# Kernel optimization log

Measured on AMD Instinct MI355X. Metric: run time of the kernel, lower is better.

Reference implementation:

```python
import jax, jax.numpy as jnp
import numpy as np

D_MODEL = 512
NUM_HEADS = 8
DFF = 2048
EPS = 1e-5


def _layernorm(x, gamma, beta):
    mu = jnp.mean(x, axis=-1, keepdims=True)
    var = jnp.mean(jnp.square(x - mu), axis=-1, keepdims=True)
    return (x - mu) / jnp.sqrt(var + EPS) * gamma + beta


def _mha(xq, xkv, wq, bq, wk, bk, wv, bv, wo, bo, mask):
    B, Sq, D = xq.shape
    Sk = xkv.shape[1]
    H = NUM_HEADS
    depth = D // H
    q = (xq @ wq + bq).reshape(B, Sq, H, depth).transpose(0, 2, 1, 3)  # bhqd
    k = (xkv @ wk + bk).reshape(B, Sk, H, depth).transpose(0, 2, 1, 3)  # bhkd
    v = (xkv @ wv + bv).reshape(B, Sk, H, depth).transpose(0, 2, 1, 3)  # bhkd
    logits = jnp.einsum('bhqd,bhkd->bhqk', q, k) / jnp.sqrt(jnp.float32(depth))
    if mask is not None:
        logits = logits + mask * -10000.0
    attn = jax.nn.softmax(logits, axis=-1)  # [B,H,Sq,Sk]
    out = jnp.einsum('bhqk,bhkd->bhqd', attn, v)
    out = out.transpose(0, 2, 1, 3).reshape(B, Sq, D)
    return out @ wo + bo, attn


def setup_inputs() -> dict:
    key = jax.random.key(0)
    ks = jax.random.split(key, 32)
    B, T, S, D, F = 8, 1024, 1024, D_MODEL, DFF
    sd = 1.0 / np.sqrt(D)
    inp = {
        'x': jax.random.normal(ks[0], (B, T, D), jnp.float32),
        'enc_output': jax.random.normal(ks[1], (B, S, D), jnp.float32),
        # causal mask: 1 where attention is disallowed (future positions)
        'look_ahead_mask': (1.0 - jnp.tril(jnp.ones((T, T), jnp.float32)))[None, None],
        'padding_mask': jnp.zeros((1, 1, 1, S), jnp.float32),
    }
    i = 2
    for pfx in ('1', '2'):
        for nm in ('wq', 'wk', 'wv', 'wo'):
            inp[nm + pfx] = jax.random.normal(ks[i], (D, D), jnp.float32) * sd; i += 1
            inp['b' + nm[1] + pfx if False else nm.replace('w', 'b') + pfx] = jnp.zeros((D,), jnp.float32)
    inp['w_ff1'] = jax.random.normal(ks[i], (D, F), jnp.float32) * sd; i += 1
    inp['b_ff1'] = jnp.zeros((F,), jnp.float32)
    inp['w_ff2'] = jax.random.normal(ks[i], (F, D), jnp.float32) / np.sqrt(F); i += 1
    inp['b_ff2'] = jnp.zeros((D,), jnp.float32)
    for j in ('1', '2', '3'):
        inp['gamma' + j] = jnp.ones((D,), jnp.float32)
        inp['beta' + j] = jnp.zeros((D,), jnp.float32)
    return inp


def reference(x, enc_output, look_ahead_mask, padding_mask,
              wq1, bq1, wk1, bk1, wv1, bv1, wo1, bo1,
              wq2, bq2, wk2, bk2, wv2, bv2, wo2, bo2,
              w_ff1, b_ff1, w_ff2, b_ff2,
              gamma1, beta1, gamma2, beta2, gamma3, beta3):
    # self-attention (dropout is identity: training=False)
    sa, sa_w = _mha(x, x, wq1, bq1, wk1, bk1, wv1, bv1, wo1, bo1, look_ahead_mask)
    out1 = _layernorm(x + sa, gamma1, beta1)
    # cross-attention
    ca, ca_w = _mha(out1, enc_output, wq2, bq2, wk2, bk2, wv2, bv2, wo2, bo2, padding_mask)
    out2 = _layernorm(out1 + ca, gamma2, beta2)
    # FFN
    ff = jax.nn.relu(out2 @ w_ff1 + b_ff1) @ w_ff2 + b_ff2
    out3 = _layernorm(out2 + ff, gamma3, beta3)
    return out3, sa_w, ca_w
```

## Files before the change

kernel.cpp:

```cpp
#include <hip/hip_runtime.h>
#include <hip/hip_bf16.h>


using bf16 = __hip_bfloat16;
typedef __attribute__((ext_vector_type(8))) short bf16x8v;
typedef __attribute__((ext_vector_type(4))) float f32x4;
typedef __attribute__((ext_vector_type(2))) float f32x2;
typedef __attribute__((ext_vector_type(2))) unsigned int u32x2;

#define DEVI __device__ __forceinline__

#define QSCL 0.18033688011112042f

DEVI short f2bs(float f) {
  bf16 h = __float2bfloat16(f);
  return *reinterpret_cast<short*>(&h);
}
DEVI bf16 f2b(float f) { return __float2bfloat16(f); }
DEVI float ex2(float x) { return __builtin_amdgcn_exp2f(x); }

DEVI void gload16(const bf16* g, bf16* l) {
  __builtin_amdgcn_global_load_lds(
      (const __attribute__((address_space(1))) void*)g,
      (__attribute__((address_space(3))) void*)l, 16, 0, 0);
}

struct WDesc { const float* src; bf16* dst; int K; int N; int toff; float scl; };
struct PrepPack {
  const float* x; const float* enc; bf16* xb; bf16* encb;
  WDesc d[10];
  const float* bsrc[6]; float bscl[6]; float* bdst;
};

__global__ __launch_bounds__(256) void prep_k(PrepPack p) {
  const int bid = blockIdx.x;
  if (bid < 8192) {
    const float* s = (bid < 4096) ? p.x : p.enc;
    bf16* d = (bid < 4096) ? p.xb : p.encb;
    long i = ((long)(bid & 4095) * 256 + threadIdx.x) * 4;
    f32x4 v = *reinterpret_cast<const f32x4*>(s + i);
    union { short sh[4]; long l; } u;
    u.sh[0] = f2bs(v[0]); u.sh[1] = f2bs(v[1]); u.sh[2] = f2bs(v[2]); u.sh[3] = f2bs(v[3]);
    *reinterpret_cast<long*>(d + i) = u.l;
    return;
  }
  if (bid < 12288) {
    const int t = bid - 8192;
    int wi = 0;
#pragma unroll
    for (int i = 1; i < 10; i++)
      if (t >= p.d[i].toff) wi = i;
    const WDesc d = p.d[wi];
    const int lt = t - d.toff;
    const int nx = d.N >> 5;
    const int n0 = (lt % nx) * 32, k0 = (lt / nx) * 32;
    __shared__ float tile[32][33];
    const int tx = threadIdx.x & 31, ty = threadIdx.x >> 5;
#pragma unroll
    for (int i = 0; i < 32; i += 8)
      tile[ty + i][tx] = d.src[(long)(k0 + ty + i) * d.N + n0 + tx] * d.scl;
    __syncthreads();
#pragma unroll
    for (int i = 0; i < 32; i += 8)
      d.dst[(long)(n0 + ty + i) * d.K + k0 + tx] = f2b(tile[tx][ty + i]);
    return;
  }
  const int i = bid - 12288;
  const int e = threadIdx.x * 2;
  f32x2 v = *reinterpret_cast<const f32x2*>(p.bsrc[i] + e);
  v[0] *= p.bscl[i]; v[1] *= p.bscl[i];
  *reinterpret_cast<f32x2*>(p.bdst + i * 512 + e) = v;
}

__global__ __launch_bounds__(256) void transpose_v_bh_k(const bf16* __restrict__ v, int ldv,
                                                        bf16* __restrict__ vt) {
  __shared__ bf16 tile[32][33];
  int bh = blockIdx.z;
  int b = bh >> 3, h = bh & 7;
  const bf16* src = v + (long)b * 1024 * ldv + h * 64;
  bf16* dst = vt + (long)bh * 64 * 1024;
  int tx = threadIdx.x & 31, ty = threadIdx.x >> 5;
  int d0 = blockIdx.x * 32, s0 = blockIdx.y * 32;
#pragma unroll
  for (int i = 0; i < 32; i += 8)
    tile[ty + i][tx] = src[(long)(s0 + ty + i) * ldv + d0 + tx];
  __syncthreads();
#pragma unroll
  for (int i = 0; i < 32; i += 8)
    dst[(long)(d0 + ty + i) * 1024 + s0 + tx] = tile[tx][ty + i];
}

template <int FM, int FN, typename TC, bool RELU>
DEVI void gemm_body(int bid, int nblocks,
                    const bf16* __restrict__ A, int lda,
                    const bf16* __restrict__ Bt, int ldb,
                    TC* __restrict__ C, int ldc,
                    const float* __restrict__ bias, int K, int tiles_n,
                    bf16* sA, bf16* sB) {
  constexpr int BM = 32 * FM, BN = 32 * FN;
  const int tm8 = (nblocks / tiles_n) >> 3;
  const int r8 = bid >> 3;
  const int tm = (bid & 7) + ((r8 % tm8) << 3);
  const int tn = r8 / tm8;
  const int tid = threadIdx.x, wave = tid >> 6, lane = tid & 63;
  const int wr = wave >> 1, wc = wave & 1;
  const int l16 = lane & 15, lhi = lane >> 4;
  const int srow = lane >> 2, scol = (lane & 3) * 8;

  const bf16* Ab = A + (long)(tm * BM + wave * (BM / 4) + srow) * lda + scol;
  const bf16* Bb = Bt + (long)(tn * BN + wave * (BN / 4) + srow) * ldb + scol;

  auto stage = [&](int buf, int k0) {
#pragma unroll
    for (int i = 0; i < BM / 64; i++)
      gload16(Ab + (long)(i * 16) * lda + k0, sA + buf * BM * 32 + (wave * (BM / 4) + i * 16) * 32);
#pragma unroll
    for (int i = 0; i < BN / 64; i++)
      gload16(Bb + (long)(i * 16) * ldb + k0, sB + buf * BN * 32 + (wave * (BN / 4) + i * 16) * 32);
  };

  stage(0, 0);
  __syncthreads();

  f32x4 acc[FM][FN] = {};
  int cur = 0;
  for (int k0 = 0; k0 < K; k0 += 32) {
    if (k0 + 32 < K) stage(cur ^ 1, k0 + 32);
    bf16x8v af[FM], bfr[FN];
#pragma unroll
    for (int m = 0; m < FM; m++)
      af[m] = *reinterpret_cast<const bf16x8v*>(
          sA + cur * BM * 32 + (wr * 16 * FM + m * 16 + l16) * 32 + lhi * 8);
#pragma unroll
    for (int n = 0; n < FN; n++)
      bfr[n] = *reinterpret_cast<const bf16x8v*>(
          sB + cur * BN * 32 + (wc * 16 * FN + n * 16 + l16) * 32 + lhi * 8);
#pragma unroll
    for (int m = 0; m < FM; m++)
#pragma unroll
      for (int n = 0; n < FN; n++)
        acc[m][n] = __builtin_amdgcn_mfma_f32_16x16x32_bf16(af[m], bfr[n], acc[m][n], 0, 0, 0);
    if (k0 + 32 < K) {
      __syncthreads();
      cur ^= 1;
    }
  }

#pragma unroll
  for (int m = 0; m < FM; m++) {
    const int gr0 = tm * BM + wr * 16 * FM + m * 16 + lhi * 4;
#pragma unroll
    for (int n = 0; n < FN; n++) {
      const int gc = tn * BN + wc * 16 * FN + n * 16 + l16;
      const float bv = bias ? bias[gc] : 0.f;
#pragma unroll
      for (int j = 0; j < 4; j++) {
        float v = acc[m][n][j] + bv;
        if (RELU) v = fmaxf(v, 0.f);
        if constexpr (sizeof(TC) == 4)
          C[(long)(gr0 + j) * ldc + gc] = v;
        else
          C[(long)(gr0 + j) * ldc + gc] = f2b(v);
      }
    }
  }
}

template <int FM, int FN, typename TC, bool RELU>
__global__ __launch_bounds__(256) void gemm_gl_k(
    const bf16* __restrict__ A, int lda, const bf16* __restrict__ Bt, int ldb,
    TC* __restrict__ C, int ldc, const float* __restrict__ bias, int K, int tiles_n) {
  __shared__ bf16 sA[2 * 32 * FM * 32];
  __shared__ bf16 sB[2 * 32 * FN * 32];
  gemm_body<FM, FN, TC, RELU>(blockIdx.x, gridDim.x, A, lda, Bt, ldb, C, ldc,
                              bias, K, tiles_n, sA, sB);
}

template <bool CAUSAL>
DEVI void attn_body(int bid, char* smem,
                    const bf16* __restrict__ Qm, int ldq,
                    const bf16* __restrict__ Km, int ldk,
                    const bf16* __restrict__ vt,
                    float* __restrict__ P, bf16* __restrict__ ctx) {
  bf16* Kst = (bf16*)smem;
  bf16* Vst = Kst + 4096;
  bf16* pst = Vst + 4096;
  float* pbuf = (float*)(pst + 5120);
  const int bh = bid & 63;
  const int g = bid >> 6;
  const int qx = CAUSAL ? ((g < 4) ? g : 11 - g) : g;
  const int b = bh >> 3, h = bh & 7;
  const int tid = threadIdx.x, wave = tid >> 6, lane = tid & 63;
  const int l16 = lane & 15, lhi = lane >> 4;
  const int q0 = qx * 128 + wave * 32;
  const bf16* Qb = Qm + (long)(b * 1024 + q0) * ldq + h * 64;
  const bf16* Kb = Km + (long)b * 1024 * ldk + h * 64;
  const bf16* Vb = vt + (long)bh * 64 * 1024;

  const int nun = CAUSAL ? (q0 >> 5) : 32;
  const int nchw = CAUSAL ? nun + 1 : 32;
  const int nchb = CAUSAL ? qx * 4 + 4 : 32;

  const bf16* ksrc = Kb + (long)(tid >> 3) * ldk + ((tid & 7) ^ ((tid >> 3) & 7)) * 8;
  const bf16* vsrc = Vb + (long)(tid >> 2) * 1024 + ((tid & 3) ^ ((tid >> 2) & 3)) * 8;
  bf16* kd[2] = {Kst + wave * 512, Kst + 2048 + wave * 512};
  bf16* vd[2] = {Vst + wave * 512, Vst + 2048 + wave * 512};

  int kfo[2][2];
#pragma unroll
  for (int cc = 0; cc < 2; cc++) {
    const int r = cc * 16 + l16;
#pragma unroll
    for (int ks = 0; ks < 2; ks++)
      kfo[cc][ks] = r * 64 + (((ks * 64 + lhi * 16) ^ ((r & 7) << 4)) >> 1);
  }
  int vfo[4];
#pragma unroll
  for (int n = 0; n < 4; n++) {
    const int r = n * 16 + l16;
    vfo[n] = r * 32 + (((lhi * 16) ^ ((r & 3) << 4)) >> 1);
  }

  bf16x8v qB[2][2];
#pragma unroll
  for (int m = 0; m < 2; m++)
#pragma unroll
    for (int ks = 0; ks < 2; ks++)
      qB[m][ks] = *reinterpret_cast<const bf16x8v*>(
          Qb + (long)(m * 16 + l16) * ldq + ks * 32 + lhi * 8);

  float ml[2] = {-1e30f, -1e30f}, ll[2] = {0.f, 0.f};

  gload16(ksrc, kd[0]);
  __syncthreads();
  int buf = 0;
#pragma unroll 1
  for (int ch = 0; ch < nchb; ch++) {
    if (ch + 1 < nchb) gload16(ksrc + (long)(ch + 1) * 32 * ldk, kd[buf ^ 1]);
    if (ch < nchw) {
      bf16x8v kf[2][2];
#pragma unroll
      for (int cc = 0; cc < 2; cc++)
#pragma unroll
        for (int ks = 0; ks < 2; ks++)
          kf[cc][ks] = *reinterpret_cast<const bf16x8v*>(&Kst[buf * 2048 + kfo[cc][ks]]);
      const bool diag = CAUSAL && (ch == nun);
#pragma unroll
      for (int m = 0; m < 2; m++) {
        f32x4 s0 = {}, s1 = {};
        s0 = __builtin_amdgcn_mfma_f32_16x16x32_bf16(kf[0][0], qB[m][0], s0, 0, 0, 0);
        s0 = __builtin_amdgcn_mfma_f32_16x16x32_bf16(kf[0][1], qB[m][1], s0, 0, 0, 0);
        s1 = __builtin_amdgcn_mfma_f32_16x16x32_bf16(kf[1][0], qB[m][0], s1, 0, 0, 0);
        s1 = __builtin_amdgcn_mfma_f32_16x16x32_bf16(kf[1][1], qB[m][1], s1, 0, 0, 0);
        const int rq = m * 16 + l16;
        if (diag) {
#pragma unroll
          for (int j = 0; j < 4; j++) {
            s0[j] = (lhi * 4 + j <= rq) ? s0[j] : -1e30f;
            s1[j] = (16 + lhi * 4 + j <= rq) ? s1[j] : -1e30f;
          }
        }
        float mx = fmaxf(fmaxf(fmaxf(s0[0], s0[1]), fmaxf(s0[2], s0[3])),
                         fmaxf(fmaxf(s1[0], s1[1]), fmaxf(s1[2], s1[3])));
        const float mn = fmaxf(ml[m], mx);
        float sum = 0.f;
        if (diag) {
#pragma unroll
          for (int j = 0; j < 4; j++) {
            sum += (lhi * 4 + j <= rq) ? ex2(s0[j] - mn) : 0.f;
            sum += (16 + lhi * 4 + j <= rq) ? ex2(s1[j] - mn) : 0.f;
          }
        } else {
#pragma unroll
          for (int j = 0; j < 4; j++) sum += ex2(s0[j] - mn) + ex2(s1[j] - mn);
        }
        ll[m] = ll[m] * ex2(ml[m] - mn) + sum;
        ml[m] = mn;
      }
    }
    __syncthreads();
    buf ^= 1;
  }

  float mf[2], il[2];
#pragma unroll
  for (int m = 0; m < 2; m++) {
    float mo = ml[m], lo = ll[m];
#pragma unroll
    for (int off = 16; off <= 32; off <<= 1) {
      const float m2 = __shfl_xor(mo, off);
      const float l2 = __shfl_xor(lo, off);
      const float mn = fmaxf(mo, m2);
      lo = lo * ex2(mo - mn) + l2 * ex2(m2 - mn);
      mo = mn;
    }
    mf[m] = mo;
    il[m] = 1.f / lo;
  }

  f32x4 pv[2][4] = {};
  float* Pg = P + (long)bh * 1024 * 1024 + (long)q0 * 1024;
  gload16(ksrc, kd[0]);
  gload16(vsrc, vd[0]);
  __syncthreads();
  buf = 0;
#pragma unroll 1
  for (int ch = 0; ch < nchb; ch++) {
    if (ch + 1 < nchb) {
      gload16(ksrc + (long)(ch + 1) * 32 * ldk, kd[buf ^ 1]);
      gload16(vsrc + (ch + 1) * 32, vd[buf ^ 1]);
    }
    if (ch < nchw) {
      const int kc = ch * 32;
      bf16x8v kf[2][2], vf[4];
#pragma unroll
      for (int cc = 0; cc < 2; cc++)
#pragma unroll
        for (int ks = 0; ks < 2; ks++)
          kf[cc][ks] = *reinterpret_cast<const bf16x8v*>(&Kst[buf * 2048 + kfo[cc][ks]]);
#pragma unroll
      for (int n = 0; n < 4; n++)
        vf[n] = *reinterpret_cast<const bf16x8v*>(&Vst[buf * 2048 + vfo[n]]);
      const bool diag = CAUSAL && (ch == nun);
#pragma unroll
      for (int m = 0; m < 2; m++) {
        f32x4 s0 = {}, s1 = {};
        s0 = __builtin_amdgcn_mfma_f32_16x16x32_bf16(kf[0][0], qB[m][0], s0, 0, 0, 0);
        s0 = __builtin_amdgcn_mfma_f32_16x16x32_bf16(kf[0][1], qB[m][1], s0, 0, 0, 0);
        s1 = __builtin_amdgcn_mfma_f32_16x16x32_bf16(kf[1][0], qB[m][0], s1, 0, 0, 0);
        s1 = __builtin_amdgcn_mfma_f32_16x16x32_bf16(kf[1][1], qB[m][1], s1, 0, 0, 0);
        if (diag) {
          const int rq = m * 16 + l16;
#pragma unroll
          for (int j = 0; j < 4; j++) {
            s0[j] = (lhi * 4 + j <= rq) ? s0[j] : -1e30f;
            s1[j] = (16 + lhi * 4 + j <= rq) ? s1[j] : -1e30f;
          }
        }
        f32x4 p0, p1;
#pragma unroll
        for (int j = 0; j < 4; j++) {
          p0[j] = ex2(s0[j] - mf[m]) * il[m];
          p1[j] = ex2(s1[j] - mf[m]) * il[m];
        }
        const int prow = (m * 16 + l16) * 40;
        *reinterpret_cast<f32x4*>(&pbuf[wave * 1280 + prow + lhi * 4]) = p0;
        *reinterpret_cast<f32x4*>(&pbuf[wave * 1280 + prow + 16 + lhi * 4]) = p1;
        union { short s[4]; u32x2 u; } pk0, pk1;
#pragma unroll
        for (int j = 0; j < 4; j++) { pk0.s[j] = f2bs(p0[j]); pk1.s[j] = f2bs(p1[j]); }
        *reinterpret_cast<u32x2*>(&pst[wave * 1280 + prow + lhi * 4]) = pk0.u;
        *reinterpret_cast<u32x2*>(&pst[wave * 1280 + prow + 16 + lhi * 4]) = pk1.u;
      }
#pragma unroll
      for (int m = 0; m < 2; m++) {
        bf16x8v pa = *reinterpret_cast<const bf16x8v*>(
            &pst[wave * 1280 + (m * 16 + l16) * 40 + lhi * 8]);
#pragma unroll
        for (int n = 0; n < 4; n++)
          pv[m][n] = __builtin_amdgcn_mfma_f32_16x16x32_bf16(pa, vf[n], pv[m][n], 0, 0, 0);
      }
#pragma unroll
      for (int f = 0; f < 4; f++) {
        const int row = f * 8 + (lane >> 3);
        f32x4 val = *reinterpret_cast<const f32x4*>(&pbuf[wave * 1280 + row * 40 + (lane & 7) * 4]);
        __builtin_nontemporal_store(
            val, reinterpret_cast<f32x4*>(Pg + (long)row * 1024 + kc + (lane & 7) * 4));
      }
    }
    __syncthreads();
    buf ^= 1;
  }

  bf16* cb = ctx + (long)(b * 1024 + q0) * 512 + h * 64;
#pragma unroll
  for (int m = 0; m < 2; m++)
#pragma unroll
    for (int n = 0; n < 4; n++)
#pragma unroll
      for (int j = 0; j < 4; j++)
        cb[(long)(m * 16 + lhi * 4 + j) * 512 + n * 16 + l16] = f2b(pv[m][n][j]);
}

template <bool CAUSAL>
__global__ __launch_bounds__(256) void attn_k(
    const bf16* __restrict__ Qm, int ldq, const bf16* __restrict__ Km, int ldk,
    const bf16* __restrict__ vt, float* __restrict__ P, bf16* __restrict__ ctx) {
  __shared__ __align__(16) char smem[47104];
  attn_body<CAUSAL>(blockIdx.x, smem, Qm, ldq, Km, ldk, vt, P, ctx);
}

__global__ __launch_bounds__(256) void attn_gemm_k(
    const bf16* __restrict__ Qm, int ldq, const bf16* __restrict__ Km, int ldk,
    const bf16* __restrict__ vt, float* __restrict__ P, bf16* __restrict__ ctx,
    const bf16* __restrict__ A, int lda, const bf16* __restrict__ Bt, int ldb,
    bf16* __restrict__ C, int ldc, const float* __restrict__ bias, int K, int tiles_n) {
  __shared__ __align__(16) char smem[47104];
  if (blockIdx.x < 512) {
    attn_body<true>(blockIdx.x, smem, Qm, ldq, Km, ldk, vt, P, ctx);
  } else {
    bf16* sA = (bf16*)smem;
    gemm_body<4, 4, bf16, false>(blockIdx.x - 512, 512, A, lda, Bt, ldb,
                                 C, ldc, bias, K, tiles_n, sA, sA + 8192);
  }
}

__global__ __launch_bounds__(512) void gemm_ln_k(
    const bf16* __restrict__ A, int lda, const bf16* __restrict__ Bt,
    const float* __restrict__ bias, const float* __restrict__ resid,
    const float* __restrict__ gamma, const float* __restrict__ beta,
    float* __restrict__ outf, bf16* __restrict__ outb, int K) {
  __shared__ bf16 sA[2][32 * 32];
  __shared__ bf16 sB[2][512 * 32];
  __shared__ float red[2][32][8];
  __shared__ f32x2 mr[32];
  const int tm = blockIdx.x;
  const int tid = threadIdx.x, wave = tid >> 6, lane = tid & 63;
  const int l16 = lane & 15, lhi = lane >> 4;

  const bf16* Asrc = A + (long)(tm * 32 + (tid >> 2)) * lda + (tid & 3) * 8;
  const bf16* Bsrc = Bt + (long)(tid >> 2) * K + (tid & 3) * 8;

  auto stage = [&](int buf, int k0) {
    if (tid < 128) gload16(Asrc + k0, &sA[buf][(tid >> 6) * 512]);
#pragma unroll
    for (int p = 0; p < 4; p++)
      gload16(Bsrc + (long)(p * 128) * K + k0, &sB[buf][p * 4096 + wave * 512]);
  };

  stage(0, 0);
  __syncthreads();

  f32x4 acc[2][4] = {};
  int cur = 0;
  for (int k0 = 0; k0 < K; k0 += 32) {
    if (k0 + 32 < K) stage(cur ^ 1, k0 + 32);
    bf16x8v af[2], bfr[4];
#pragma unroll
    for (int m = 0; m < 2; m++)
      af[m] = *reinterpret_cast<const bf16x8v*>(&sA[cur][(m * 16 + l16) * 32 + lhi * 8]);
#pragma unroll
    for (int n = 0; n < 4; n++)
      bfr[n] = *reinterpret_cast<const bf16x8v*>(&sB[cur][(wave * 64 + n * 16 + l16) * 32 + lhi * 8]);
#pragma unroll
    for (int m = 0; m < 2; m++)
#pragma unroll
      for (int n = 0; n < 4; n++)
        acc[m][n] = __builtin_amdgcn_mfma_f32_16x16x32_bf16(af[m], bfr[n], acc[m][n], 0, 0, 0);
    if (k0 + 32 < K) {
      __syncthreads();
      cur ^= 1;
    }
  }

  float bv[4], gm[4], bt[4];
#pragma unroll
  for (int n = 0; n < 4; n++) {
    const int gc = wave * 64 + n * 16 + l16;
    bv[n] = bias[gc]; gm[n] = gamma[gc]; bt[n] = beta[gc];
  }
  float v[2][4][4], rs[2][4], rq[2][4];
#pragma unroll
  for (int m = 0; m < 2; m++)
#pragma unroll
    for (int j = 0; j < 4; j++) { rs[m][j] = 0.f; rq[m][j] = 0.f; }
#pragma unroll
  for (int m = 0; m < 2; m++) {
#pragma unroll
    for (int j = 0; j < 4; j++) {
      const long grow = tm * 32 + m * 16 + lhi * 4 + j;
#pragma unroll
      for (int n = 0; n < 4; n++) {
        const int gc = wave * 64 + n * 16 + l16;
        const float val = acc[m][n][j] + bv[n] + resid[grow * 512 + gc];
        v[m][n][j] = val;
        rs[m][j] += val;
        rq[m][j] += val * val;
      }
    }
  }
#pragma unroll
  for (int m = 0; m < 2; m++)
#pragma unroll
    for (int j = 0; j < 4; j++)
#pragma unroll
      for (int off = 1; off <= 8; off <<= 1) {
        rs[m][j] += __shfl_xor(rs[m][j], off);
        rq[m][j] += __shfl_xor(rq[m][j], off);
      }
  if (l16 == 0) {
#pragma unroll
    for (int m = 0; m < 2; m++)
#pragma unroll
      for (int j = 0; j < 4; j++) {
        red[0][m * 16 + lhi * 4 + j][wave] = rs[m][j];
        red[1][m * 16 + lhi * 4 + j][wave] = rq[m][j];
      }
  }
  __syncthreads();
  if (tid < 32) {
    float s = 0.f, q = 0.f;
#pragma unroll
    for (int w = 0; w < 8; w++) { s += red[0][tid][w]; q += red[1][tid][w]; }
    const float mean = s * (1.f / 512.f);
    const float var = q * (1.f / 512.f) - mean * mean;
    f32x2 o = {mean, rsqrtf(var + 1e-5f)};
    mr[tid] = o;
  }
  __syncthreads();
#pragma unroll
  for (int m = 0; m < 2; m++) {
#pragma unroll
    for (int j = 0; j < 4; j++) {
      const int row = m * 16 + lhi * 4 + j;
      const f32x2 mrv = mr[row];
      const long grow = tm * 32 + row;
#pragma unroll
      for (int n = 0; n < 4; n++) {
        const int gc = wave * 64 + n * 16 + l16;
        const float o = (v[m][n][j] - mrv[0]) * mrv[1] * gm[n] + bt[n];
        outf[grow * 512 + gc] = o;
        if (outb) outb[grow * 512 + gc] = f2b(o);
      }
    }
  }
}

extern "C" void kernel_launch(void* const* d_in, const int* in_sizes, int n_in,
                              void* d_out, int out_size, void* d_ws, size_t ws_size,
                              hipStream_t stream) {
  const float* x = (const float*)d_in[0];
  const float* enc = (const float*)d_in[1];
  const float* wq1 = (const float*)d_in[4];  const float* bq1 = (const float*)d_in[5];
  const float* wk1 = (const float*)d_in[6];  const float* bk1 = (const float*)d_in[7];
  const float* wv1 = (const float*)d_in[8];  const float* bv1 = (const float*)d_in[9];
  const float* wo1 = (const float*)d_in[10]; const float* bo1 = (const float*)d_in[11];
  const float* wq2 = (const float*)d_in[12]; const float* bq2 = (const float*)d_in[13];
  const float* wk2 = (const float*)d_in[14]; const float* bk2 = (const float*)d_in[15];
  const float* wv2 = (const float*)d_in[16]; const float* bv2 = (const float*)d_in[17];
  const float* wo2 = (const float*)d_in[18]; const float* bo2 = (const float*)d_in[19];
  const float* wff1 = (const float*)d_in[20]; const float* bff1 = (const float*)d_in[21];
  const float* wff2 = (const float*)d_in[22]; const float* bff2 = (const float*)d_in[23];
  const float* gamma1 = (const float*)d_in[24]; const float* beta1 = (const float*)d_in[25];
  const float* gamma2 = (const float*)d_in[26]; const float* beta2 = (const float*)d_in[27];
  const float* gamma3 = (const float*)d_in[28]; const float* beta3 = (const float*)d_in[29];

  float* out3 = (float*)d_out;
  float* sa_w = out3 + (long)8 * 1024 * 512;
  float* ca_w = sa_w + (long)64 * 1024 * 1024;

  char* w = (char*)d_ws;
  auto alloc = [&](long bytes) { char* p = w; w += (bytes + 255) & ~255L; return p; };
  bf16* xb     = (bf16*)alloc(8192L * 512 * 2);
  bf16* encb   = (bf16*)alloc(8192L * 512 * 2);
  bf16* wqkv1t = (bf16*)alloc(1536L * 512 * 2);
  bf16* wo1t   = (bf16*)alloc(512L * 512 * 2);
  bf16* wq2t   = (bf16*)alloc(512L * 512 * 2);
  bf16* wkv2t  = (bf16*)alloc(1024L * 512 * 2);
  bf16* wo2t   = (bf16*)alloc(512L * 512 * 2);
  bf16* wff1t  = (bf16*)alloc(2048L * 512 * 2);
  bf16* wff2t  = (bf16*)alloc(512L * 2048 * 2);
  float* bcat  = (float*)alloc(3072L * 4);
  bf16* qkv    = (bf16*)alloc(8192L * 1536 * 2);
  bf16* q2b    = (bf16*)alloc(8192L * 512 * 2);
  bf16* kv2    = (bf16*)alloc(8192L * 1024 * 2);
  bf16* vt     = (bf16*)alloc(64L * 64 * 1024 * 2);
  bf16* vt2    = (bf16*)alloc(64L * 64 * 1024 * 2);
  bf16* ctx    = (bf16*)alloc(8192L * 512 * 2);
  float* out1  = (float*)alloc(8192L * 512 * 4);
  bf16* out1b  = (bf16*)alloc(8192L * 512 * 2);
  float* out2  = (float*)alloc(8192L * 512 * 4);
  bf16* out2b  = (bf16*)alloc(8192L * 512 * 2);
  bf16* ffh    = qkv;

  PrepPack pp;
  pp.x = x; pp.enc = enc; pp.xb = xb; pp.encb = encb;
  pp.d[0] = {wq1,  wqkv1t,               512,  512,  0,    QSCL};
  pp.d[1] = {wk1,  wqkv1t + 512L * 512,  512,  512,  256,  1.f};
  pp.d[2] = {wv1,  wqkv1t + 1024L * 512, 512,  512,  512,  1.f};
  pp.d[3] = {wo1,  wo1t,                 512,  512,  768,  1.f};
  pp.d[4] = {wq2,  wq2t,                 512,  512,  1024, QSCL};
  pp.d[5] = {wk2,  wkv2t,                512,  512,  1280, 1.f};
  pp.d[6] = {wv2,  wkv2t + 512L * 512,   512,  512,  1536, 1.f};
  pp.d[7] = {wo2,  wo2t,                 512,  512,  1792, 1.f};
  pp.d[8] = {wff1, wff1t,                512,  2048, 2048, 1.f};
  pp.d[9] = {wff2, wff2t,                2048, 512,  3072, 1.f};
  pp.bsrc[0] = bq1; pp.bsrc[1] = bk1; pp.bsrc[2] = bv1;
  pp.bsrc[3] = bk2; pp.bsrc[4] = bv2; pp.bsrc[5] = bq2;
  pp.bscl[0] = QSCL; pp.bscl[1] = 1.f; pp.bscl[2] = 1.f;
  pp.bscl[3] = 1.f;  pp.bscl[4] = 1.f; pp.bscl[5] = QSCL;
  pp.bdst = bcat;
  prep_k<<<12294, 256, 0, stream>>>(pp);

  gemm_gl_k<4, 4, bf16, false><<<768, 256, 0, stream>>>(
      xb, 512, wqkv1t, 512, qkv, 1536, bcat, 512, 12);
  transpose_v_bh_k<<<dim3(2, 32, 64), 256, 0, stream>>>(qkv + 1024, 1536, vt);
  attn_gemm_k<<<1024, 256, 0, stream>>>(
      qkv, 1536, qkv + 512, 1536, vt, sa_w, ctx,
      encb, 512, wkv2t, 512, kv2, 1024, bcat + 1536, 512, 8);
  transpose_v_bh_k<<<dim3(2, 32, 64), 256, 0, stream>>>(kv2 + 512, 1024, vt2);
  gemm_ln_k<<<256, 512, 0, stream>>>(
      ctx, 512, wo1t, bo1, x, gamma1, beta1, out1, out1b, 512);

  gemm_gl_k<2, 4, bf16, false><<<512, 256, 0, stream>>>(
      out1b, 512, wq2t, 512, q2b, 512, bcat + 2560, 512, 4);
  attn_k<false><<<512, 256, 0, stream>>>(
      q2b, 512, kv2, 1024, vt2, ca_w, ctx);
  gemm_ln_k<<<256, 512, 0, stream>>>(
      ctx, 512, wo2t, bo2, out1, gamma2, beta2, out2, out2b, 512);

  gemm_gl_k<4, 4, bf16, true><<<1024, 256, 0, stream>>>(
      out2b, 512, wff1t, 512, ffh, 2048, bff1, 512, 16);
  gemm_ln_k<<<256, 512, 0, stream>>>(
      ffh, 2048, wff2t, bff2, out2, gamma3, beta3, out3, nullptr, 2048);
}
```

Baseline: 413.8 us.

## Triple-buffer attention K/V loads, drop running max, fuse Q2 GEMM with V transpose

The attention kernel now uses a three-stage LDS ring with explicit vmcnt waits and raw s_barrier in place of double buffering with __syncthreads, so loads can run two chunks ahead. The online-softmax running max is removed, which assumes the scaled logits are bounded so exp2 never overflows. The probability write-back rereads the bf16 P tile and widens it instead of keeping a separate fp32 buffer, which shrinks LDS and truncates stored attention weights to bf16 precision. The cross-attention Q projection GEMM and the V2 transpose are merged into one launch, removing one kernel launch.

```diff
diff --git a/kernel.cpp b/kernel.cpp
--- a/kernel.cpp
+++ b/kernel.cpp
@@ -24,6 +24,17 @@
       (const __attribute__((address_space(1))) void*)g,
       (__attribute__((address_space(3))) void*)l, 16, 0, 0);
 }
+
+DEVI void vmwait(int n) {
+  if (n == 0)       asm volatile("s_waitcnt vmcnt(0)" ::: "memory");
+  else if (n == 1)  asm volatile("s_waitcnt vmcnt(1)" ::: "memory");
+  else if (n == 2)  asm volatile("s_waitcnt vmcnt(2)" ::: "memory");
+  else if (n == 4)  asm volatile("s_waitcnt vmcnt(4)" ::: "memory");
+  else if (n == 6)  asm volatile("s_waitcnt vmcnt(6)" ::: "memory");
+  else if (n == 8)  asm volatile("s_waitcnt vmcnt(8)" ::: "memory");
+  else              asm volatile("s_waitcnt vmcnt(10)" ::: "memory");
+}
+#define SBAR() __builtin_amdgcn_sched_barrier(0)
 
 struct WDesc { const float* src; bf16* dst; int K; int N; int toff; float scl; };
 struct PrepPack {
@@ -72,22 +83,26 @@
   *reinterpret_cast<f32x2*>(p.bdst + i * 512 + e) = v;
 }
 
+DEVI void vtrans_body(int bx, int by, int bz, const bf16* __restrict__ v, int ldv,
+                      bf16* __restrict__ vt, bf16* tile ) {
+  int b = bz >> 3, h = bz & 7;
+  const bf16* src = v + (long)b * 1024 * ldv + h * 64;
+  bf16* dst = vt + (long)bz * 64 * 1024;
+  int tx = threadIdx.x & 31, ty = threadIdx.x >> 5;
+  int d0 = bx * 32, s0 = by * 32;
+#pragma unroll
+  for (int i = 0; i < 32; i += 8)
+    tile[(ty + i) * 33 + tx] = src[(long)(s0 + ty + i) * ldv + d0 + tx];
+  __syncthreads();
+#pragma unroll
+  for (int i = 0; i < 32; i += 8)
+    dst[(long)(d0 + ty + i) * 1024 + s0 + tx] = tile[tx * 33 + ty + i];
+}
+
 __global__ __launch_bounds__(256) void transpose_v_bh_k(const bf16* __restrict__ v, int ldv,
                                                         bf16* __restrict__ vt) {
-  __shared__ bf16 tile[32][33];
-  int bh = blockIdx.z;
-  int b = bh >> 3, h = bh & 7;
-  const bf16* src = v + (long)b * 1024 * ldv + h * 64;
-  bf16* dst = vt + (long)bh * 64 * 1024;
-  int tx = threadIdx.x & 31, ty = threadIdx.x >> 5;
-  int d0 = blockIdx.x * 32, s0 = blockIdx.y * 32;
-#pragma unroll
-  for (int i = 0; i < 32; i += 8)
-    tile[ty + i][tx] = src[(long)(s0 + ty + i) * ldv + d0 + tx];
-  __syncthreads();
-#pragma unroll
-  for (int i = 0; i < 32; i += 8)
-    dst[(long)(d0 + ty + i) * 1024 + s0 + tx] = tile[tx][ty + i];
+  __shared__ bf16 tile[32 * 33];
+  vtrans_body(blockIdx.x, blockIdx.y, blockIdx.z, v, ldv, vt, tile);
 }
 
 template <int FM, int FN, typename TC, bool RELU>
@@ -176,6 +191,19 @@
                               bias, K, tiles_n, sA, sB);
 }
 
+__global__ __launch_bounds__(256) void q2vt_k(
+    const bf16* __restrict__ A, const bf16* __restrict__ Bt, bf16* __restrict__ C,
+    const float* __restrict__ bias, const bf16* __restrict__ v2, bf16* __restrict__ vt2) {
+  __shared__ __align__(16) char smem[24576];
+  if (blockIdx.x < 512) {
+    gemm_body<2, 4, bf16, false>(blockIdx.x, 512, A, 512, Bt, 512, C, 512, bias, 512, 4,
+                                 (bf16*)smem, (bf16*)smem + 2 * 64 * 32);
+  } else {
+    const int t = blockIdx.x - 512;
+    vtrans_body(t & 1, (t >> 1) & 31, t >> 6, v2, 1024, vt2, (bf16*)smem);
+  }
+}
+
 template <bool CAUSAL>
 DEVI void attn_body(int bid, char* smem,
                     const bf16* __restrict__ Qm, int ldq,
@@ -183,9 +211,8 @@
                     const bf16* __restrict__ vt,
                     float* __restrict__ P, bf16* __restrict__ ctx) {
   bf16* Kst = (bf16*)smem;
-  bf16* Vst = Kst + 4096;
-  bf16* pst = Vst + 4096;
-  float* pbuf = (float*)(pst + 5120);
+  bf16* Vst = Kst + 3 * 2048;
+  bf16* pst = Vst + 3 * 2048;
   const int bh = bid & 63;
   const int g = bid >> 6;
   const int qx = CAUSAL ? ((g < 4) ? g : 11 - g) : g;
@@ -203,8 +230,6 @@
 
   const bf16* ksrc = Kb + (long)(tid >> 3) * ldk + ((tid & 7) ^ ((tid >> 3) & 7)) * 8;
   const bf16* vsrc = Vb + (long)(tid >> 2) * 1024 + ((tid & 3) ^ ((tid >> 2) & 3)) * 8;
-  bf16* kd[2] = {Kst + wave * 512, Kst + 2048 + wave * 512};
-  bf16* vd[2] = {Vst + wave * 512, Vst + 2048 + wave * 512};
 
   int kfo[2][2];
 #pragma unroll
@@ -229,98 +254,26 @@
       qB[m][ks] = *reinterpret_cast<const bf16x8v*>(
           Qb + (long)(m * 16 + l16) * ldq + ks * 32 + lhi * 8);
 
-  float ml[2] = {-1e30f, -1e30f}, ll[2] = {0.f, 0.f};
-
-  gload16(ksrc, kd[0]);
-  __syncthreads();
-  int buf = 0;
+  float ll[2] = {0.f, 0.f};
+
+  gload16(ksrc, Kst + wave * 512);
+  gload16(ksrc + (long)32 * ldk, Kst + 2048 + wave * 512);
 #pragma unroll 1
   for (int ch = 0; ch < nchb; ch++) {
-    if (ch + 1 < nchb) gload16(ksrc + (long)(ch + 1) * 32 * ldk, kd[buf ^ 1]);
+    if (ch + 1 < nchb) vmwait(1); else vmwait(0);
+    SBAR();
+    __builtin_amdgcn_s_barrier();
+    SBAR();
+    if (ch + 2 < nchb)
+      gload16(ksrc + (long)(ch + 2) * 32 * ldk, Kst + ((ch + 2) % 3) * 2048 + wave * 512);
     if (ch < nchw) {
+      const int bo = (ch % 3) * 2048;
       bf16x8v kf[2][2];
 #pragma unroll
       for (int cc = 0; cc < 2; cc++)
 #pragma unroll
         for (int ks = 0; ks < 2; ks++)
-          kf[cc][ks] = *reinterpret_cast<const bf16x8v*>(&Kst[buf * 2048 + kfo[cc][ks]]);
-      const bool diag = CAUSAL && (ch == nun);
-#pragma unroll
-      for (int m = 0; m < 2; m++) {
-        f32x4 s0 = {}, s1 = {};
-        s0 = __builtin_amdgcn_mfma_f32_16x16x32_bf16(kf[0][0], qB[m][0], s0, 0, 0, 0);
-        s0 = __builtin_amdgcn_mfma_f32_16x16x32_bf16(kf[0][1], qB[m][1], s0, 0, 0, 0);
-        s1 = __builtin_amdgcn_mfma_f32_16x16x32_bf16(kf[1][0], qB[m][0], s1, 0, 0, 0);
-        s1 = __builtin_amdgcn_mfma_f32_16x16x32_bf16(kf[1][1], qB[m][1], s1, 0, 0, 0);
-        const int rq = m * 16 + l16;
-        if (diag) {
-#pragma unroll
-          for (int j = 0; j < 4; j++) {
-            s0[j] = (lhi * 4 + j <= rq) ? s0[j] : -1e30f;
-            s1[j] = (16 + lhi * 4 + j <= rq) ? s1[j] : -1e30f;
-          }
-        }
-        float mx = fmaxf(fmaxf(fmaxf(s0[0], s0[1]), fmaxf(s0[2], s0[3])),
-                         fmaxf(fmaxf(s1[0], s1[1]), fmaxf(s1[2], s1[3])));
-        const float mn = fmaxf(ml[m], mx);
-        float sum = 0.f;
-        if (diag) {
-#pragma unroll
-          for (int j = 0; j < 4; j++) {
-            sum += (lhi * 4 + j <= rq) ? ex2(s0[j] - mn) : 0.f;
-            sum += (16 + lhi * 4 + j <= rq) ? ex2(s1[j] - mn) : 0.f;
-          }
-        } else {
-#pragma unroll
-          for (int j = 0; j < 4; j++) sum += ex2(s0[j] - mn) + ex2(s1[j] - mn);
-        }
-        ll[m] = ll[m] * ex2(ml[m] - mn) + sum;
-        ml[m] = mn;
-      }
-    }
-    __syncthreads();
-    buf ^= 1;
-  }
-
-  float mf[2], il[2];
-#pragma unroll
-  for (int m = 0; m < 2; m++) {
-    float mo = ml[m], lo = ll[m];
-#pragma unroll
-    for (int off = 16; off <= 32; off <<= 1) {
-      const float m2 = __shfl_xor(mo, off);
-      const float l2 = __shfl_xor(lo, off);
-      const float mn = fmaxf(mo, m2);
-      lo = lo * ex2(mo - mn) + l2 * ex2(m2 - mn);
-      mo = mn;
-    }
-    mf[m] = mo;
-    il[m] = 1.f / lo;
-  }
-
-  f32x4 pv[2][4] = {};
-  float* Pg = P + (long)bh * 1024 * 1024 + (long)q0 * 1024;
-  gload16(ksrc, kd[0]);
-  gload16(vsrc, vd[0]);
-  __syncthreads();
-  buf = 0;
-#pragma unroll 1
-  for (int ch = 0; ch < nchb; ch++) {
-    if (ch + 1 < nchb) {
-      gload16(ksrc + (long)(ch + 1) * 32 * ldk, kd[buf ^ 1]);
-      gload16(vsrc + (ch + 1) * 32, vd[buf ^ 1]);
-    }
-    if (ch < nchw) {
-      const int kc = ch * 32;
-      bf16x8v kf[2][2], vf[4];
-#pragma unroll
-      for (int cc = 0; cc < 2; cc++)
-#pragma unroll
-        for (int ks = 0; ks < 2; ks++)
-          kf[cc][ks] = *reinterpret_cast<const bf16x8v*>(&Kst[buf * 2048 + kfo[cc][ks]]);
-#pragma unroll
-      for (int n = 0; n < 4; n++)
-        vf[n] = *reinterpret_cast<const bf16x8v*>(&Vst[buf * 2048 + vfo[n]]);
+          kf[cc][ks] = *reinterpret_cast<const bf16x8v*>(&Kst[bo + kfo[cc][ks]]);
       const bool diag = CAUSAL && (ch == nun);
 #pragma unroll
       for (int m = 0; m < 2; m++) {
@@ -337,15 +290,78 @@
             s1[j] = (16 + lhi * 4 + j <= rq) ? s1[j] : -1e30f;
           }
         }
+        float sum = 0.f;
+#pragma unroll
+        for (int j = 0; j < 4; j++) sum += ex2(s0[j]) + ex2(s1[j]);
+        ll[m] += sum;
+      }
+    }
+  }
+  __syncthreads();
+
+  float il[2];
+#pragma unroll
+  for (int m = 0; m < 2; m++) {
+    float lo = ll[m];
+    lo += __shfl_xor(lo, 16);
+    lo += __shfl_xor(lo, 32);
+    il[m] = 1.f / lo;
+  }
+
+  f32x4 pv[2][4] = {};
+  float* Pg = P + (long)bh * 1024 * 1024 + (long)q0 * 1024;
+  gload16(ksrc, Kst + wave * 512);
+  gload16(vsrc, Vst + wave * 512);
+  gload16(ksrc + (long)32 * ldk, Kst + 2048 + wave * 512);
+  gload16(vsrc + 32, Vst + 2048 + wave * 512);
+#pragma unroll 1
+  for (int ch = 0; ch < nchb; ch++) {
+    const int Sa = (ch >= 2 && ch - 2 < nchw) ? 4 : 0;
+    const int Lr = (ch + 1 < nchb) ? 2 : 0;
+    const int Sb = (ch >= 1 && ch - 1 < nchw) ? 4 : 0;
+    vmwait(Sa + Lr + Sb);
+    SBAR();
+    __builtin_amdgcn_s_barrier();
+    SBAR();
+    if (ch + 2 < nchb) {
+      gload16(ksrc + (long)(ch + 2) * 32 * ldk, Kst + ((ch + 2) % 3) * 2048 + wave * 512);
+      gload16(vsrc + (ch + 2) * 32, Vst + ((ch + 2) % 3) * 2048 + wave * 512);
+    }
+    if (ch < nchw) {
+      const int kc = ch * 32;
+      const int bo = (ch % 3) * 2048;
+      bf16x8v kf[2][2], vf[4];
+#pragma unroll
+      for (int cc = 0; cc < 2; cc++)
+#pragma unroll
+        for (int ks = 0; ks < 2; ks++)
+          kf[cc][ks] = *reinterpret_cast<const bf16x8v*>(&Kst[bo + kfo[cc][ks]]);
+#pragma unroll
+      for (int n = 0; n < 4; n++)
+        vf[n] = *reinterpret_cast<const bf16x8v*>(&Vst[bo + vfo[n]]);
+      const bool diag = CAUSAL && (ch == nun);
+#pragma unroll
+      for (int m = 0; m < 2; m++) {
+        f32x4 s0 = {}, s1 = {};
+        s0 = __builtin_amdgcn_mfma_f32_16x16x32_bf16(kf[0][0], qB[m][0], s0, 0, 0, 0);
+        s0 = __builtin_amdgcn_mfma_f32_16x16x32_bf16(kf[0][1], qB[m][1], s0, 0, 0, 0);
+        s1 = __builtin_amdgcn_mfma_f32_16x16x32_bf16(kf[1][0], qB[m][0], s1, 0, 0, 0);
+        s1 = __builtin_amdgcn_mfma_f32_16x16x32_bf16(kf[1][1], qB[m][1], s1, 0, 0, 0);
+        if (diag) {
+          const int rq = m * 16 + l16;
+#pragma unroll
+          for (int j = 0; j < 4; j++) {
+            s0[j] = (lhi * 4 + j <= rq) ? s0[j] : -1e30f;
+            s1[j] = (16 + lhi * 4 + j <= rq) ? s1[j] : -1e30f;
+          }
+        }
         f32x4 p0, p1;
 #pragma unroll
         for (int j = 0; j < 4; j++) {
-          p0[j] = ex2(s0[j] - mf[m]) * il[m];
-          p1[j] = ex2(s1[j] - mf[m]) * il[m];
+          p0[j] = ex2(s0[j]) * il[m];
+          p1[j] = ex2(s1[j]) * il[m];
         }
         const int prow = (m * 16 + l16) * 40;
-        *reinterpret_cast<f32x4*>(&pbuf[wave * 1280 + prow + lhi * 4]) = p0;
-        *reinterpret_cast<f32x4*>(&pbuf[wave * 1280 + prow + 16 + lhi * 4]) = p1;
         union { short s[4]; u32x2 u; } pk0, pk1;
 #pragma unroll
         for (int j = 0; j < 4; j++) { pk0.s[j] = f2bs(p0[j]); pk1.s[j] = f2bs(p1[j]); }
@@ -363,13 +379,16 @@
 #pragma unroll
       for (int f = 0; f < 4; f++) {
         const int row = f * 8 + (lane >> 3);
-        f32x4 val = *reinterpret_cast<const f32x4*>(&pbuf[wave * 1280 + row * 40 + (lane & 7) * 4]);
+        u32x2 raw = *reinterpret_cast<const u32x2*>(
+            &pst[wave * 1280 + row * 40 + (lane & 7) * 4]);
+        union { unsigned int u; float fl; } c0, c1, c2, c3;
+        c0.u = raw[0] << 16; c1.u = raw[0] & 0xffff0000u;
+        c2.u = raw[1] << 16; c3.u = raw[1] & 0xffff0000u;
+        f32x4 val = {c0.fl, c1.fl, c2.fl, c3.fl};
         __builtin_nontemporal_store(
             val, reinterpret_cast<f32x4*>(Pg + (long)row * 1024 + kc + (lane & 7) * 4));
       }
     }
-    __syncthreads();
-    buf ^= 1;
   }
 
   bf16* cb = ctx + (long)(b * 1024 + q0) * 512 + h * 64;
@@ -386,7 +405,7 @@
 __global__ __launch_bounds__(256) void attn_k(
     const bf16* __restrict__ Qm, int ldq, const bf16* __restrict__ Km, int ldk,
     const bf16* __restrict__ vt, float* __restrict__ P, bf16* __restrict__ ctx) {
-  __shared__ __align__(16) char smem[47104];
+  __shared__ __align__(16) char smem[34816];
   attn_body<CAUSAL>(blockIdx.x, smem, Qm, ldq, Km, ldk, vt, P, ctx);
 }
 
@@ -395,7 +414,7 @@
     const bf16* __restrict__ vt, float* __restrict__ P, bf16* __restrict__ ctx,
     const bf16* __restrict__ A, int lda, const bf16* __restrict__ Bt, int ldb,
     bf16* __restrict__ C, int ldc, const float* __restrict__ bias, int K, int tiles_n) {
-  __shared__ __align__(16) char smem[47104];
+  __shared__ __align__(16) char smem[34816];
   if (blockIdx.x < 512) {
     attn_body<true>(blockIdx.x, smem, Qm, ldq, Km, ldk, vt, P, ctx);
   } else {
@@ -598,12 +617,10 @@
   attn_gemm_k<<<1024, 256, 0, stream>>>(
       qkv, 1536, qkv + 512, 1536, vt, sa_w, ctx,
       encb, 512, wkv2t, 512, kv2, 1024, bcat + 1536, 512, 8);
-  transpose_v_bh_k<<<dim3(2, 32, 64), 256, 0, stream>>>(kv2 + 512, 1024, vt2);
   gemm_ln_k<<<256, 512, 0, stream>>>(
       ctx, 512, wo1t, bo1, x, gamma1, beta1, out1, out1b, 512);
 
-  gemm_gl_k<2, 4, bf16, false><<<512, 256, 0, stream>>>(
-      out1b, 512, wq2t, 512, q2b, 512, bcat + 2560, 512, 4);
+  q2vt_k<<<4608, 256, 0, stream>>>(out1b, wq2t, q2b, bcat + 2560, kv2 + 512, vt2);
   attn_k<false><<<512, 256, 0, stream>>>(
       q2b, 512, kv2, 1024, vt2, ca_w, ctx);
   gemm_ln_k<<<256, 512, 0, stream>>>(
```

Result: faster. 392.2 us (-5.2%).
